# Optimization experiments

Measured on AMD Instinct MI355X. Metric: run time of the kernel, lower is better.

The kernel has to match this reference:

```python
import jax, jax.numpy as jnp
import numpy as np

IN_F = 2048
OUT_F = 2048
BS = 64  # block_size
NIB = IN_F // BS   # 32 in-blocks
NOB = OUT_F // BS  # 32 out-blocks


def setup_inputs() -> dict:
    key = jax.random.key(0)
    k_x, k_s1, k_s2, k_m = jax.random.split(key, 4)
    bound = 1.0 / np.sqrt(BS)
    x = jax.random.normal(k_x, (4, 4096, IN_F), dtype=jnp.float32)
    stage1 = jax.random.uniform(k_s1, (NIB * BS, BS), minval=-bound, maxval=bound, dtype=jnp.float32)
    stage2 = jax.random.uniform(k_s2, (NOB * BS, BS), minval=-bound, maxval=bound, dtype=jnp.float32)
    mix_w = jax.random.normal(k_m, (NOB * BS, NIB * BS), dtype=jnp.float32) / np.sqrt(IN_F)
    return {"x": x, "stage1": stage1, "stage2": stage2, "mix_w": mix_w}


def _blockdiag(x, weight, num_blocks):
    # x: [..., num_blocks*BS]; weight: [num_blocks*BS, BS] viewed as [g, c, d]
    shape = x.shape[:-1]
    xg = x.reshape(-1, num_blocks, BS)
    w = weight.reshape(num_blocks, BS, BS)
    y = jnp.einsum('ngc,gcd->ngd', xg, w)
    return y.reshape(*shape, num_blocks * BS)


def _shuffle(x):
    # interpret last dim as [BS, NIB], transpose to [NIB, BS]
    shape = x.shape[:-1]
    return x.reshape(-1, BS, NIB).transpose(0, 2, 1).reshape(*shape, NIB * BS)


def reference(x, stage1, stage2, mix_w):
    h = _blockdiag(x, stage1, NIB)          # [B,S,IN_F]
    h = _shuffle(h)                          # [B,S,IN_F]
    h = jnp.einsum('bsi,oi->bso', h, mix_w)  # dense mix, no bias
    return _blockdiag(h, stage2, NOB)        # [B,S,OUT_F]
```

## Files before the change

### kernel.cpp

```cpp
#include <hip/hip_runtime.h>
#include <stdint.h>

#define IN_F 2048
#define OUT_F 2048
#define MTOK 16384

typedef __attribute__((ext_vector_type(8))) __bf16 bf16x8;
typedef __attribute__((ext_vector_type(4))) float f32x4;
typedef __attribute__((ext_vector_type(4))) unsigned short us4;

typedef const __attribute__((address_space(1))) void g_void;
typedef __attribute__((address_space(3))) void l_void;

__device__ __forceinline__ void async16(void* lds, const void* g) {
    __builtin_amdgcn_global_load_lds((g_void*)(uintptr_t)g, (l_void*)(uintptr_t)lds, 16, 0, 0);
}

__device__ __forceinline__ unsigned short f2bf(float x) {
    union { float f; uint32_t u; } v; v.f = x;
    uint32_t r = v.u + 0x7fffu + ((v.u >> 16) & 1u);
    return (unsigned short)(r >> 16);
}

__global__ __launch_bounds__(256) void k_perm(
    const float* __restrict__ MW, float* __restrict__ Bpf) {
    __shared__ float buf[2112];
    const int t = threadIdx.x;
    const float* src = MW + (size_t)blockIdx.x * 2048;
    float* dst = Bpf + (size_t)blockIdx.x * 2048;
#pragma unroll
    for (int q = 0; q < 2; ++q) {
        int id4 = q * 256 + t;
        float4 v = *(const float4*)(src + id4 * 4);
        int i = id4 * 4;
        int b = i + (i >> 5);
        buf[b] = v.x; buf[b + 1] = v.y; buf[b + 2] = v.z; buf[b + 3] = v.w;
    }
    __syncthreads();
#pragma unroll
    for (int q = 0; q < 8; ++q) {
        int j = q * 256 + t;
        int i = ((j & 31) << 6) | (j >> 5);
        dst[j] = buf[i + (i >> 5)];
    }
}

#define FP 68

__global__ __launch_bounds__(256) void k_fold(
    const float* __restrict__ s1, const float* __restrict__ s2,
    const float* __restrict__ Bpf, unsigned short* __restrict__ Bb) {
    __shared__ float B0[64 * FP];
    __shared__ float B1[64 * FP];
    const int t = threadIdx.x;
    const int g  = blockIdx.x & 31;
    const int rt = blockIdx.x >> 5;
    const int l = t & 15, h = t >> 4;

#pragma unroll
    for (int q = 0; q < 4; ++q) {
        int id = q * 256 + t;
        int c = id >> 4, d4 = id & 15;
        *(float4*)&B0[c * FP + d4 * 4] =
            *(const float4*)(s1 + (size_t)(g * 64 + c) * 64 + d4 * 4);
    }
#pragma unroll
    for (int q = 0; q < 4; ++q) {
        int id = q * 256 + t;
        int o = id >> 4, d4 = id & 15;
        *(float4*)&B1[o * FP + d4 * 4] =
            *(const float4*)(Bpf + (size_t)(rt * 64 + o) * 2048 + g * 64 + d4 * 4);
    }
    __syncthreads();

    float acc[4][4];
#pragma unroll
    for (int i = 0; i < 4; ++i)
#pragma unroll
        for (int j = 0; j < 4; ++j) acc[i][j] = 0.f;
    {
        const int co = l * 4, oo = h * 4;
#pragma unroll
        for (int dc = 0; dc < 16; ++dc) {
            const int dce = (dc + l) & 15;
            float4 bv[4], wv[4];
#pragma unroll
            for (int i = 0; i < 4; ++i) bv[i] = *(const float4*)&B1[(oo + i) * FP + dce * 4];
#pragma unroll
            for (int j = 0; j < 4; ++j) wv[j] = *(const float4*)&B0[(co + j) * FP + dce * 4];
#pragma unroll
            for (int i = 0; i < 4; ++i)
#pragma unroll
                for (int j = 0; j < 4; ++j)
                    acc[i][j] += bv[i].x * wv[j].x + bv[i].y * wv[j].y
                               + bv[i].z * wv[j].z + bv[i].w * wv[j].w;
        }
    }
    __syncthreads();

    {
        const int co = l * 4, oo = h * 4;
#pragma unroll
        for (int j = 0; j < 4; ++j) {
            float4 v; v.x = acc[0][j]; v.y = acc[1][j]; v.z = acc[2][j]; v.w = acc[3][j];
            *(float4*)&B0[(co + j) * FP + oo] = v;
        }
    }
#pragma unroll
    for (int q = 0; q < 4; ++q) {
        int id = q * 256 + t;
        int c2 = id >> 4, d4 = id & 15;
        *(float4*)&B1[c2 * FP + d4 * 4] =
            *(const float4*)(s2 + (size_t)(rt * 64 + c2) * 64 + d4 * 4);
    }
    __syncthreads();

    {
        const int d2o = l * 4, cco = h * 4;
#pragma unroll
        for (int i = 0; i < 4; ++i)
#pragma unroll
            for (int j = 0; j < 4; ++j) acc[i][j] = 0.f;
#pragma unroll
        for (int kc = 0; kc < 16; ++kc) {
            const int kce = (kc + l) & 15;
            float4 wv4[4], mv[4];
#pragma unroll
            for (int s = 0; s < 4; ++s) wv4[s] = *(const float4*)&B1[(kce * 4 + s) * FP + d2o];
#pragma unroll
            for (int j = 0; j < 4; ++j) mv[j] = *(const float4*)&B0[(cco + j) * FP + kce * 4];
#pragma unroll
            for (int i = 0; i < 4; ++i)
#pragma unroll
                for (int j = 0; j < 4; ++j)
                    acc[i][j] += wv4[0][i] * mv[j].x + wv4[1][i] * mv[j].y
                               + wv4[2][i] * mv[j].z + wv4[3][i] * mv[j].w;
        }
#pragma unroll
        for (int i = 0; i < 4; ++i) {
            us4 o;
            o[0] = f2bf(acc[i][0]); o[1] = f2bf(acc[i][1]);
            o[2] = f2bf(acc[i][2]); o[3] = f2bf(acc[i][3]);
            *(us4*)(Bb + (size_t)(rt * 64 + d2o + i) * 2048 + g * 64 + cco) = o;
        }
    }
}

__global__ __launch_bounds__(256) void k_convert(
    const float* __restrict__ X, unsigned short* __restrict__ Xb) {
    const int gid = blockIdx.x * 256 + threadIdx.x;
    const float4* src = (const float4*)X;
    us4* dst = (us4*)Xb;
#pragma unroll
    for (int k = 0; k < 16; ++k) {
        int idx = k * (2048 * 256) + gid;
        float4 v = src[idx];
        us4 o;
        o[0] = f2bf(v.x); o[1] = f2bf(v.y); o[2] = f2bf(v.z); o[3] = f2bf(v.w);
        dst[idx] = o;
    }
}

__global__ __launch_bounds__(256, 2) void k_gemm(
    const unsigned short* __restrict__ A, const unsigned short* __restrict__ B,
    float* __restrict__ C) {
    __shared__ unsigned short smem[16384];
    unsigned short* As = smem;
    unsigned short* Bs = smem + 8192;
    const int t = threadIdx.x;
    const int lane = t & 63, wave = t >> 6;
    const int quad = lane >> 4, l16 = lane & 15;
    const int mw = wave & 1, nw = wave >> 1;
    const int orig = blockIdx.y * 128 + blockIdx.x;
    const int lin = (orig & 7) * 256 + (orig >> 3);
    const int m0 = (lin >> 4) * 128;
    const int n0 = (lin & 15) * 128;
    const int rr = t >> 3, chunk = t & 7;
    const int gsw = (chunk ^ (rr & 7)) * 8;
    const int lsw = l16 & 7;

    f32x4 acc[4][4];
#pragma unroll
    for (int i = 0; i < 4; ++i)
#pragma unroll
        for (int j = 0; j < 4; ++j) acc[i][j] = (f32x4)0.f;

    for (int kb = 0; kb < IN_F; kb += 64) {
#pragma unroll
        for (int q = 0; q < 4; ++q) {
            int r = q * 32 + rr;
            async16((char*)As + (size_t)(q * 4096 + t * 16),
                    A + (size_t)(m0 + r) * IN_F + kb + gsw);
            async16((char*)Bs + (size_t)(q * 4096 + t * 16),
                    B + (size_t)(n0 + r) * IN_F + kb + gsw);
        }
        __syncthreads();
#pragma unroll
        for (int ks = 0; ks < 2; ++ks) {
            bf16x8 af[4], bfr[4];
#pragma unroll
            for (int i = 0; i < 4; ++i)
                af[i] = *(const bf16x8*)(As + (mw * 64 + i * 16 + l16) * 64
                                            + (((ks * 4 + quad) ^ lsw) * 8));
#pragma unroll
            for (int j = 0; j < 4; ++j)
                bfr[j] = *(const bf16x8*)(Bs + (nw * 64 + j * 16 + l16) * 64
                                             + (((ks * 4 + quad) ^ lsw) * 8));
#pragma unroll
            for (int i = 0; i < 4; ++i)
#pragma unroll
                for (int j = 0; j < 4; ++j)
                    acc[i][j] = __builtin_amdgcn_mfma_f32_16x16x32_bf16(af[i], bfr[j], acc[i][j], 0, 0, 0);
        }
        __syncthreads();
    }

#pragma unroll
    for (int i = 0; i < 4; ++i)
#pragma unroll
        for (int j = 0; j < 4; ++j) {
            float* Cp = C + (size_t)(m0 + mw * 64 + i * 16 + quad * 4) * OUT_F
                          + (n0 + nw * 64 + j * 16 + l16);
#pragma unroll
            for (int r = 0; r < 4; ++r) Cp[(size_t)r * OUT_F] = acc[i][j][r];
        }
}

extern "C" void kernel_launch(void* const* d_in, const int* in_sizes, int n_in,
                              void* d_out, int out_size, void* d_ws, size_t ws_size,
                              hipStream_t stream) {
    const float* x  = (const float*)d_in[0];
    const float* s1 = (const float*)d_in[1];
    const float* s2 = (const float*)d_in[2];
    const float* mw = (const float*)d_in[3];
    float* out = (float*)d_out;

    char* ws = (char*)d_ws;
    unsigned short* Xb  = (unsigned short*)ws;
    float*          Bpf = (float*)ws;
    unsigned short* Bb  = (unsigned short*)(ws + (size_t)MTOK * IN_F * 2);

    k_perm<<<2048, 256, 0, stream>>>(mw, Bpf);
    k_fold<<<1024, 256, 0, stream>>>(s1, s2, Bpf, Bb);
    k_convert<<<2048, 256, 0, stream>>>(x, Xb);
    k_gemm<<<dim3(128, 16), 256, 0, stream>>>(Xb, Bb, out);
}
```

Baseline: 399.1 us.

## Enlarge GEMM tiles to 256x256 with double-buffered async LDS prefetch

The bf16 GEMM now uses 256x256 output tiles, 512-thread blocks of 8 waves and a 1D grid with a remapped block order. The next K-tile of A and B is loaded asynchronously into a second LDS buffer while MFMAs run on the current one, which removes one barrier per iteration and overlaps global loads with compute. Wave priority is raised around the MFMA bursts. The cost is 128KB of LDS per block, which limits occupancy to one block per CU, and twice as many accumulator registers per wave.

```diff
diff --git a/kernel.cpp b/kernel.cpp
--- a/kernel.cpp
+++ b/kernel.cpp
@@ -161,66 +161,88 @@
     }
 }
 
-__global__ __launch_bounds__(256, 2) void k_gemm(
+__global__ __launch_bounds__(512, 2) void k_gemm(
     const unsigned short* __restrict__ A, const unsigned short* __restrict__ B,
     float* __restrict__ C) {
-    __shared__ unsigned short smem[16384];
-    unsigned short* As = smem;
-    unsigned short* Bs = smem + 8192;
+    __shared__ unsigned short smem[65536];
+    char* lds = (char*)smem;
     const int t = threadIdx.x;
-    const int lane = t & 63, wave = t >> 6;
+    const int lane = t & 63;
+    const int wave = t >> 6;
     const int quad = lane >> 4, l16 = lane & 15;
-    const int mw = wave & 1, nw = wave >> 1;
-    const int orig = blockIdx.y * 128 + blockIdx.x;
-    const int lin = (orig & 7) * 256 + (orig >> 3);
-    const int m0 = (lin >> 4) * 128;
-    const int n0 = (lin & 15) * 128;
+    const int wm = wave & 1, wn = wave >> 1;
+    const int orig = blockIdx.x;
+    const int lin = (orig & 7) * 64 + (orig >> 3);
+    const int m0 = (lin >> 3) * 256;
+    const int n0 = (lin & 7) * 256;
     const int rr = t >> 3, chunk = t & 7;
     const int gsw = (chunk ^ (rr & 7)) * 8;
     const int lsw = l16 & 7;
 
-    f32x4 acc[4][4];
-#pragma unroll
-    for (int i = 0; i < 4; ++i)
+    f32x4 acc[8][4];
+#pragma unroll
+    for (int i = 0; i < 8; ++i)
 #pragma unroll
         for (int j = 0; j < 4; ++j) acc[i][j] = (f32x4)0.f;
 
-    for (int kb = 0; kb < IN_F; kb += 64) {
-#pragma unroll
-        for (int q = 0; q < 4; ++q) {
-            int r = q * 32 + rr;
-            async16((char*)As + (size_t)(q * 4096 + t * 16),
-                    A + (size_t)(m0 + r) * IN_F + kb + gsw);
-            async16((char*)Bs + (size_t)(q * 4096 + t * 16),
-                    B + (size_t)(n0 + r) * IN_F + kb + gsw);
-        }
-        __syncthreads();
+#pragma unroll
+    for (int q = 0; q < 4; ++q)
+        async16(lds + q * 8192 + t * 16,
+                A + (size_t)(m0 + q * 64 + rr) * IN_F + 0 + gsw);
+#pragma unroll
+    for (int q = 0; q < 4; ++q)
+        async16(lds + 65536 + q * 8192 + t * 16,
+                B + (size_t)(n0 + q * 64 + rr) * IN_F + 0 + gsw);
+    __syncthreads();
+
+    for (int kt = 0; kt < 32; ++kt) {
+        const int c = kt & 1;
+        const unsigned short* As = (const unsigned short*)(lds + c * 32768);
+        const unsigned short* Bs = (const unsigned short*)(lds + 65536 + c * 32768);
+        char* An = lds + (c ^ 1) * 32768;
+        char* Bn = lds + 65536 + (c ^ 1) * 32768;
+        const int kbn = (kt + 1) * 64;
+
+        if (kt < 31) {
+#pragma unroll
+            for (int q = 0; q < 4; ++q)
+                async16(An + q * 8192 + t * 16,
+                        A + (size_t)(m0 + q * 64 + rr) * IN_F + kbn + gsw);
+        }
 #pragma unroll
         for (int ks = 0; ks < 2; ++ks) {
-            bf16x8 af[4], bfr[4];
-#pragma unroll
-            for (int i = 0; i < 4; ++i)
-                af[i] = *(const bf16x8*)(As + (mw * 64 + i * 16 + l16) * 64
+            if (ks == 1 && kt < 31) {
+#pragma unroll
+                for (int q = 0; q < 4; ++q)
+                    async16(Bn + q * 8192 + t * 16,
+                            B + (size_t)(n0 + q * 64 + rr) * IN_F + kbn + gsw);
+            }
+            bf16x8 af[8], bfr[4];
+#pragma unroll
+            for (int i = 0; i < 8; ++i)
+                af[i] = *(const bf16x8*)(As + (wm * 128 + i * 16 + l16) * 64
                                             + (((ks * 4 + quad) ^ lsw) * 8));
 #pragma unroll
             for (int j = 0; j < 4; ++j)
-                bfr[j] = *(const bf16x8*)(Bs + (nw * 64 + j * 16 + l16) * 64
+                bfr[j] = *(const bf16x8*)(Bs + (wn * 64 + j * 16 + l16) * 64
                                              + (((ks * 4 + quad) ^ lsw) * 8));
-#pragma unroll
-            for (int i = 0; i < 4; ++i)
+            __builtin_amdgcn_s_setprio(1);
+#pragma unroll
+            for (int i = 0; i < 8; ++i)
 #pragma unroll
                 for (int j = 0; j < 4; ++j)
                     acc[i][j] = __builtin_amdgcn_mfma_f32_16x16x32_bf16(af[i], bfr[j], acc[i][j], 0, 0, 0);
+            __builtin_amdgcn_s_setprio(0);
         }
         __syncthreads();
     }
 
 #pragma unroll
-    for (int i = 0; i < 4; ++i)
+    for (int i = 0; i < 8; ++i)
 #pragma unroll
         for (int j = 0; j < 4; ++j) {
-            float* Cp = C + (size_t)(m0 + mw * 64 + i * 16 + quad * 4) * OUT_F
-                          + (n0 + nw * 64 + j * 16 + l16);
+            float* Cp = C + (size_t)(m0 + wm * 128 + i * 16 + quad * 4) * OUT_F
+                          + (n0 + wn * 64 + j * 16 + l16);
 #pragma unroll
             for (int r = 0; r < 4; ++r) Cp[(size_t)r * OUT_F] = acc[i][j][r];
         }
@@ -243,5 +265,5 @@
     k_perm<<<2048, 256, 0, stream>>>(mw, Bpf);
     k_fold<<<1024, 256, 0, stream>>>(s1, s2, Bpf, Bb);
     k_convert<<<2048, 256, 0, stream>>>(x, Xb);
-    k_gemm<<<dim3(128, 16), 256, 0, stream>>>(Xb, Bb, out);
-}
+    k_gemm<<<512, 512, 0, stream>>>(Xb, Bb, out);
+}
```

New measurement: 381.3 us. 4.5% less time.
